# Performance work log

Measured on AMD Instinct MI355X. Metric: run time of the kernel, lower is better.

Reference implementation:

```python
import jax, jax.numpy as jnp
import numpy as np
from jax import lax

IMG = 256; STRIDE = 16; FH = FW = 16; A = 9
SCALES = (32.0, 64.0, 128.0); RATIOS = (0.5, 1.0, 2.0)
N_PROP = 2000; CROP = 14
C_BB = 64


def _conv(x, w, b, stride=1, pad='SAME'):
    y = lax.conv_general_dilated(x, w, (stride, stride), pad,
                                 dimension_numbers=('NCHW', 'OIHW', 'NCHW'))
    return y + b[None, :, None, None]


def _anchors():
    s = jnp.array(SCALES, jnp.float32); r = jnp.array(RATIOS, jnp.float32)
    sr = jnp.stack(jnp.meshgrid(s, r, indexing='ij'), -1).reshape(-1, 2)  # [A,2]
    ws = sr[:, 0] * jnp.sqrt(sr[:, 1]); hs = sr[:, 0] / jnp.sqrt(sr[:, 1])
    cy = (jnp.arange(FH, dtype=jnp.float32) + 0.5) * STRIDE
    cx = (jnp.arange(FW, dtype=jnp.float32) + 0.5) * STRIDE
    cy, cx = jnp.meshgrid(cy, cx, indexing='ij')
    cy = cy[..., None]; cx = cx[..., None]  # [FH,FW,1]
    return jnp.stack([cx - ws / 2, cy - hs / 2, cx + ws / 2, cy + hs / 2], -1).reshape(-1, 4)


def _decode(deltas, anchors):
    w = anchors[:, 2] - anchors[:, 0]; h = anchors[:, 3] - anchors[:, 1]
    cx = anchors[:, 0] + 0.5 * w; cy = anchors[:, 1] + 0.5 * h
    ncx = cx + deltas[:, 0] * w; ncy = cy + deltas[:, 1] * h
    nw = w * jnp.exp(deltas[:, 2]); nh = h * jnp.exp(deltas[:, 3])
    return jnp.stack([ncx - 0.5 * nw, ncy - 0.5 * nh, ncx + 0.5 * nw, ncy + 0.5 * nh], -1)


def _clip(b):
    lim = jnp.float32(IMG - 1)
    return jnp.stack([jnp.clip(b[:, 0], 0, lim), jnp.clip(b[:, 1], 0, lim),
                      jnp.clip(b[:, 2], 0, lim), jnp.clip(b[:, 3], 0, lim)], -1)


def _nms(boxes, scores, thr):
    # greedy NMS; returns order (desc score) and keep mask in sorted order
    order = jnp.argsort(-scores)
    b = boxes[order]
    area = jnp.maximum(b[:, 2] - b[:, 0], 0) * jnp.maximum(b[:, 3] - b[:, 1], 0)
    xx1 = jnp.maximum(b[:, None, 0], b[None, :, 0]); yy1 = jnp.maximum(b[:, None, 1], b[None, :, 1])
    xx2 = jnp.minimum(b[:, None, 2], b[None, :, 2]); yy2 = jnp.minimum(b[:, None, 3], b[None, :, 3])
    inter = jnp.maximum(xx2 - xx1, 0) * jnp.maximum(yy2 - yy1, 0)
    iou = inter / (area[:, None] + area[None, :] - inter + 1e-8)
    n = boxes.shape[0]; idx = jnp.arange(n)
    def body(i, keep):
        return keep & ~(keep[i] & (iou[i] > thr) & (idx > i))
    keep = lax.fori_loop(0, n, body, jnp.ones(n, dtype=bool))
    return order, keep


def _crop_resize(feat, nboxes):
    # feat [C,FH,FW]; nboxes [N,4] normalized (y1,x1,y2,x2) -> [N,C,CROP,CROP]
    t = jnp.arange(CROP, dtype=jnp.float32) / (CROP - 1)
    def one(bx):
        y1, x1, y2, x2 = bx
        fy = (y1 + (y2 - y1) * t) * (FH - 1)
        fx = (x1 + (x2 - x1) * t) * (FW - 1)
        y0 = jnp.clip(jnp.floor(fy), 0, FH - 1).astype(jnp.int32); y1i = jnp.clip(y0 + 1, 0, FH - 1)
        x0 = jnp.clip(jnp.floor(fx), 0, FW - 1).astype(jnp.int32); x1i = jnp.clip(x0 + 1, 0, FW - 1)
        wy = (fy - y0.astype(fy.dtype))[:, None]   # [CROP,1]
        wx = (fx - x0.astype(fx.dtype))[None, :]   # [1,CROP]
        g = lambda yi, xi: feat[:, yi[:, None], xi[None, :]]  # [C,CROP,CROP]
        top = g(y0, x0) * (1 - wx) + g(y0, x1i) * wx
        bot = g(y1i, x0) * (1 - wx) + g(y1i, x1i) * wx
        return top * (1 - wy) + bot * wy
    return jax.vmap(one)(nboxes)


def _forward(x, w_bb, b_bb, w_rpn, b_rpn, w_cls, b_cls, w_box, b_box,
             w_fc1, b_fc1, w_fc2, b_fc2, w_rcls, b_rcls, w_rbox, b_rbox,
             w_m1, b_m1, w_m2, b_m2):
    anchors = _anchors()
    feat = jax.nn.relu(_conv(x, w_bb, b_bb, stride=STRIDE, pad='VALID'))  # [1,C,16,16]
    h = jax.nn.relu(_conv(feat, w_rpn, b_rpn))
    rpn_logits = _conv(h, w_cls, b_cls)[0].reshape(A, 2, FH, FW).transpose(2, 3, 0, 1).reshape(-1, 2)
    rpn_deltas = _conv(h, w_box, b_box)[0].reshape(A, 4, FH, FW).transpose(2, 3, 0, 1).reshape(-1, 4)
    scores = jax.nn.softmax(rpn_logits, -1)[:, 1]
    boxes = _clip(_decode(rpn_deltas, anchors))
    order, keep = _nms(boxes, scores, 0.5)
    n = boxes.shape[0]
    prio = jnp.where(keep, 0, 1) * n + jnp.arange(n)   # kept first, in score order
    sel = jnp.argsort(prio)[:N_PROP]
    valid = keep[sel]
    proposals = jnp.where(valid[:, None], boxes[order][sel], 0.0)  # [N_PROP,4] xyxy
    nb = jnp.stack([proposals[:, 1], proposals[:, 0], proposals[:, 3], proposals[:, 2]], -1) / (IMG - 1)
    crops = _crop_resize(feat[0], nb)                  # [N_PROP,C,14,14]
    pooled = crops.reshape(N_PROP, C_BB, 7, 2, 7, 2).max(axis=(3, 5))
    flat = pooled.reshape(N_PROP, -1)
    h1 = jax.nn.relu(flat @ w_fc1 + b_fc1)
    h2 = jax.nn.relu(h1 @ w_fc2 + b_fc2)
    rcnn_logits = h2 @ w_rcls + b_rcls                 # [N_PROP,2]
    rcnn_deltas = h2 @ w_rbox + b_rbox                 # [N_PROP,4]
    m = jax.nn.relu(_conv(crops, w_m1, b_m1))
    rcnn_masks = _conv(m, w_m2, b_m2)                  # [N_PROP,1,14,14]
    det_scores = jax.nn.softmax(rcnn_logits, -1)[:, 1]
    dets = _clip(_decode(rcnn_deltas, proposals))
    s2 = jnp.where(valid, det_scores, -1.0)
    order2, keep2 = _nms(dets, s2, 0.3)
    keep2 = keep2 & valid[order2]
    final_dets = jnp.where(keep2[:, None], dets[order2], 0.0)
    final_scores = jnp.where(keep2, det_scores[order2], 0.0)
    final_masks = jax.nn.sigmoid(rcnn_masks[order2][:, 0]) * keep2[:, None, None].astype(crops.dtype)
    return (rpn_logits, rpn_deltas, proposals, anchors, rcnn_logits, rcnn_deltas,
            rcnn_masks, final_dets, final_masks, final_scores, keep2)


def setup_inputs() -> dict:
    key = jax.random.key(0)
    ks = jax.random.split(key, 24)
    rn = lambda k, sh, s: jax.random.normal(k, sh, dtype=jnp.float32) * s
    C = C_BB
    return {
        'x': rn(ks[0], (1, 3, IMG, IMG), 1.0),
        'w_bb': rn(ks[1], (C, 3, STRIDE, STRIDE), 0.03), 'b_bb': jnp.zeros((C,), jnp.float32),
        'w_rpn': rn(ks[2], (C, C, 3, 3), 0.05), 'b_rpn': jnp.zeros((C,), jnp.float32),
        'w_cls': rn(ks[3], (2 * A, C, 1, 1), 0.05), 'b_cls': jnp.zeros((2 * A,), jnp.float32),
        'w_box': rn(ks[4], (4 * A, C, 1, 1), 0.05), 'b_box': jnp.zeros((4 * A,), jnp.float32),
        'w_fc1': rn(ks[5], (C * 7 * 7, 512), 0.02), 'b_fc1': jnp.zeros((512,), jnp.float32),
        'w_fc2': rn(ks[6], (512, 512), 0.04), 'b_fc2': jnp.zeros((512,), jnp.float32),
        'w_rcls': rn(ks[7], (512, 2), 0.05), 'b_rcls': jnp.zeros((2,), jnp.float32),
        'w_rbox': rn(ks[8], (512, 4), 0.05), 'b_rbox': jnp.zeros((4,), jnp.float32),
        'w_m1': rn(ks[9], (C, C, 3, 3), 0.05), 'b_m1': jnp.zeros((C,), jnp.float32),
        'w_m2': rn(ks[10], (1, C, 1, 1), 0.05), 'b_m2': jnp.zeros((1,), jnp.float32),
    }


def reference(x, w_bb, b_bb, w_rpn, b_rpn, w_cls, b_cls, w_box, b_box,
              w_fc1, b_fc1, w_fc2, b_fc2, w_rcls, b_rcls, w_rbox, b_rbox,
              w_m1, b_m1, w_m2, b_m2):
    return _forward(x, w_bb, b_bb, w_rpn, b_rpn, w_cls, b_cls, w_box, b_box,
                    w_fc1, b_fc1, w_fc2, b_fc2, w_rcls, b_rcls, w_rbox, b_rbox,
                    w_m1, b_m1, w_m2, b_m2)
```

## Files before the change

### kernel.cpp

```cpp
#include <hip/hip_runtime.h>
#include <math.h>

typedef unsigned long long u64;
typedef unsigned short u16;
typedef __attribute__((ext_vector_type(8))) short bf16x8;
typedef __attribute__((ext_vector_type(4))) float f32x4;
typedef __attribute__((ext_vector_type(16))) float f32x16;

#define N_ANCH 2304
#define NP     2000
#define W1     36
#define W2     32

#define O_RPN_LOGITS   0
#define O_RPN_DELTAS   4608
#define O_PROPOSALS    13824
#define O_ANCHORS      21824
#define O_RCNN_LOGITS  31040
#define O_RCNN_DELTAS  35040
#define O_RCNN_MASKS   43040
#define O_FINAL_DETS   435040
#define O_FINAL_MASKS  443040
#define O_FINAL_SCORES 835040
#define O_KEEP2        837040

__device__ __forceinline__ u16 f2bf(float f) {
    unsigned int x = __float_as_uint(f);
    unsigned int r = x + 0x7fffu + ((x >> 16) & 1u);
    return (u16)(r >> 16);
}

__global__ __launch_bounds__(256) void bb_conv(const float* __restrict__ x,
    const float* __restrict__ w, const float* __restrict__ b,
    float* __restrict__ feat, float* __restrict__ feat_tf)
{
    __shared__ __align__(16) float ws_[768];
    int c = blockIdx.x;
    for (int e = threadIdx.x; e < 192; e += 256)
        ((float4*)ws_)[e] = ((const float4*)(w + c*768))[e];
    __syncthreads();
    int fy = threadIdx.x >> 4, fx = threadIdx.x & 15;
    float acc = b[c];
    for (int ic = 0; ic < 3; ++ic)
        for (int ky = 0; ky < 16; ++ky) {
            const float* xr = x + (size_t)(ic*256 + fy*16+ky)*256 + fx*16;
            const float* wr = ws_ + ic*256 + ky*16;
            float xv[16];
            *(float4*)&xv[0]  = *(const float4*)(xr);
            *(float4*)&xv[4]  = *(const float4*)(xr+4);
            *(float4*)&xv[8]  = *(const float4*)(xr+8);
            *(float4*)&xv[12] = *(const float4*)(xr+12);
            #pragma unroll
            for (int kx = 0; kx < 16; ++kx) acc += xv[kx]*wr[kx];
        }
    float v = fmaxf(acc, 0.f);
    feat[c*256 + threadIdx.x] = v;
    feat_tf[threadIdx.x*64 + c] = v;
}

__global__ __launch_bounds__(256) void rpn_conv(const float* __restrict__ feat,
    const float* __restrict__ w, const float* __restrict__ b, float* __restrict__ h)
{
    __shared__ __align__(16) float f[16384];
    __shared__ __align__(16) float ws_[576];
    int c = blockIdx.x;
    for (int e = threadIdx.x; e < 4096; e += 256)
        ((float4*)f)[e] = ((const float4*)feat)[e];
    for (int e = threadIdx.x; e < 144; e += 256)
        ((float4*)ws_)[e] = ((const float4*)(w + c*576))[e];
    __syncthreads();
    int fy = threadIdx.x >> 4, fx = threadIdx.x & 15;
    float acc = b[c];
    for (int ic = 0; ic < 64; ++ic) {
        const float* fc = f + ic*256;
        const float* wc = ws_ + ic*9;
        #pragma unroll
        for (int dy = 0; dy < 3; ++dy) {
            int y = fy + dy - 1;
            if (y < 0 || y > 15) continue;
            #pragma unroll
            for (int dx = 0; dx < 3; ++dx) {
                int xx = fx + dx - 1;
                if (xx < 0 || xx > 15) continue;
                acc += fc[y*16+xx]*wc[dy*3+dx];
            }
        }
    }
    h[c*256 + threadIdx.x] = fmaxf(acc, 0.f);
}

__global__ __launch_bounds__(256) void heads_rpn(const float* __restrict__ hbuf,
    const float* __restrict__ w_cls, const float* __restrict__ b_cls,
    const float* __restrict__ w_box, const float* __restrict__ b_box,
    float* __restrict__ out_logits, float* __restrict__ out_deltas,
    float* __restrict__ out_anchors,
    float* __restrict__ scores, float* __restrict__ boxes)
{
    int idx = blockIdx.x*256 + threadIdx.x;
    if (idx >= N_ANCH) return;
    int fy = idx / 144, r = idx % 144, fx = r / 9, a = r % 9;
    int pix = fy*16 + fx;
    float l0 = b_cls[a*2+0], l1 = b_cls[a*2+1];
    float d0 = b_box[a*4+0], d1 = b_box[a*4+1], d2 = b_box[a*4+2], d3 = b_box[a*4+3];
    const float* wc0 = w_cls + (a*2+0)*64;
    const float* wc1 = w_cls + (a*2+1)*64;
    const float* wb0 = w_box + (a*4+0)*64;
    const float* wb1 = w_box + (a*4+1)*64;
    const float* wb2 = w_box + (a*4+2)*64;
    const float* wb3 = w_box + (a*4+3)*64;
    for (int c = 0; c < 64; ++c) {
        float hv = hbuf[c*256 + pix];
        l0 += hv*wc0[c]; l1 += hv*wc1[c];
        d0 += hv*wb0[c]; d1 += hv*wb1[c]; d2 += hv*wb2[c]; d3 += hv*wb3[c];
    }
    out_logits[idx*2+0] = l0; out_logits[idx*2+1] = l1;
    out_deltas[idx*4+0] = d0; out_deltas[idx*4+1] = d1;
    out_deltas[idx*4+2] = d2; out_deltas[idx*4+3] = d3;
    float mx = fmaxf(l0,l1);
    float e0 = expf(l0-mx), e1 = expf(l1-mx);
    scores[idx] = e1/(e0+e1);
    float SC = (a/3 == 0) ? 32.f : ((a/3 == 1) ? 64.f : 128.f);
    float RT = (a%3 == 0) ? 0.5f : ((a%3 == 1) ? 1.f : 2.f);
    float wsz = SC*sqrtf(RT), hsz = SC/sqrtf(RT);
    float cx = (fx+0.5f)*16.f, cy = (fy+0.5f)*16.f;
    float ax1 = cx - wsz*0.5f, ay1 = cy - hsz*0.5f;
    float ax2 = cx + wsz*0.5f, ay2 = cy + hsz*0.5f;
    out_anchors[idx*4+0]=ax1; out_anchors[idx*4+1]=ay1;
    out_anchors[idx*4+2]=ax2; out_anchors[idx*4+3]=ay2;
    float aw = ax2-ax1, ah = ay2-ay1;
    float acx = ax1 + 0.5f*aw, acy = ay1 + 0.5f*ah;
    float ncx = acx + d0*aw, ncy = acy + d1*ah;
    float nw = aw*expf(d2), nh = ah*expf(d3);
    float x1 = ncx - 0.5f*nw, y1 = ncy - 0.5f*nh;
    float x2 = ncx + 0.5f*nw, y2 = ncy + 0.5f*nh;
    const float lim = 255.f;
    x1 = fminf(fmaxf(x1,0.f),lim); y1 = fminf(fmaxf(y1,0.f),lim);
    x2 = fminf(fmaxf(x2,0.f),lim); y2 = fminf(fmaxf(y2,0.f),lim);
    boxes[idx*4+0]=x1; boxes[idx*4+1]=y1; boxes[idx*4+2]=x2; boxes[idx*4+3]=y2;
}

__global__ __launch_bounds__(256) void rank_part(const float* __restrict__ score,
    int* __restrict__ parts, int n)
{
    __shared__ __align__(16) float sj[256];
    int it = blockIdx.x, jt = blockIdx.y;
    int i = it*256 + threadIdx.x;
    int j0 = jt*256;
    int jj = j0 + threadIdx.x;
    sj[threadIdx.x] = (jj < n) ? score[jj] : 0.f;
    __syncthreads();
    if (i >= n) return;
    float si = score[i];
    int jmax = min(256, n - j0);
    int cnt = 0;
    const float4* s4 = (const float4*)sj;
    int q4 = jmax >> 2;
    for (int q = 0; q < q4; ++q) {
        float4 v = s4[q];
        int j = j0 + q*4;
        cnt += (v.x > si) || (v.x == si && (j+0) < i);
        cnt += (v.y > si) || (v.y == si && (j+1) < i);
        cnt += (v.z > si) || (v.z == si && (j+2) < i);
        cnt += (v.w > si) || (v.w == si && (j+3) < i);
    }
    parts[(size_t)jt*n + i] = cnt;
}

__global__ __launch_bounds__(256) void rank_scatter(const int* __restrict__ parts,
    int* __restrict__ order, int n, int S)
{
    int i = blockIdx.x*256 + threadIdx.x;
    if (i >= n) return;
    int r = 0;
    for (int s = 0; s < S; ++s) r += parts[(size_t)s*n + i];
    order[r] = i;
}

__global__ __launch_bounds__(256) void gather_sorted(const float4* __restrict__ boxes,
    const int* __restrict__ order, float4* __restrict__ sb, float* __restrict__ sa, int n)
{
    int i = blockIdx.x*256 + threadIdx.x;
    if (i >= n) return;
    float4 b = boxes[order[i]];
    sb[i] = b;
    sa[i] = fmaxf(b.z-b.x, 0.f)*fmaxf(b.w-b.y, 0.f);
}

__global__ __launch_bounds__(256) void iou_mask(const float4* __restrict__ sb,
    const float* __restrict__ sa, int n, int ntotal, int words, float thr,
    u64* __restrict__ mask)
{
    int gid = blockIdx.x*256 + threadIdx.x;
    if (gid >= ntotal*words) return;
    int i = gid / words, w = gid % words;
    if (i >= n) { mask[(size_t)i*words + w] = 0; return; }
    float4 bi = sb[i]; float ai = sa[i];
    u64 m = 0;
    int j0 = w*64;
    for (int bb = 0; bb < 64; ++bb) {
        int j = j0 + bb;
        if (j > i && j < n) {
            float4 bj = sb[j];
            float xx1 = fmaxf(bi.x, bj.x), yy1 = fmaxf(bi.y, bj.y);
            float xx2 = fminf(bi.z, bj.z), yy2 = fminf(bi.w, bj.w);
            float inter = fmaxf(xx2-xx1, 0.f)*fmaxf(yy2-yy1, 0.f);
            float iou = inter / (ai + sa[j] - inter + 1e-8f);
            if (iou > thr) m |= 1ULL << bb;
        }
    }
    mask[(size_t)i*words + w] = m;
}

__global__ __launch_bounds__(256, 1) void nms_scan_wg(const u64* __restrict__ mask,
    int nblk, int words, u64* __restrict__ remout)
{
    __shared__ u64 rem_lds[64];
    __shared__ u64 diagS[64];
    __shared__ u64 pslot[8*64];
    int t = threadIdx.x;
    int ngrp = 256 / words;
    int g = t / words, c = t % words;
    bool pactive = (g < ngrp);
    int gg = min(g, ngrp - 1);
    if (t < 64) {
        rem_lds[t] = ~0ULL;
        diagS[t] = mask[(size_t)t*words + 0];
    }
    __syncthreads();
    for (int b = 0; b < nblk; ++b) {
        const u64* blockbase = mask + (size_t)(64*b)*words;
        u64 vals[10];
        int rows[10];
        #pragma unroll
        for (int k = 0; k < 10; ++k) {
            int r = min(gg + k*ngrp, 63);
            rows[k] = r;
            vals[k] = blockbase[(size_t)r*words + c];
        }
        u64 dnext = mask[(size_t)(64*(b+1) + (t & 63))*words + min(b+1, words-1)];
        u64 mydia = diagS[t & 63];
        u64 nz = __ballot(mydia != 0ULL);
        u64 cur = rem_lds[b];
        u64 pend = cur & nz;
        unsigned mlo = (unsigned)mydia;
        unsigned mhi = (unsigned)(mydia >> 32);
        while (pend) {
            int i = __ffsll((unsigned long long)pend) - 1;
            unsigned lo = __builtin_amdgcn_readlane((int)mlo, i);
            unsigned hi = __builtin_amdgcn_readlane((int)mhi, i);
            u64 dia = ((u64)hi << 32) | lo;
            cur  &= ~dia;
            pend &= ~dia;
            pend &= pend - 1;
        }
        u64 partial = ~0ULL;
        #pragma unroll
        for (int k = 0; k < 10; ++k) {
            bool al = (cur >> rows[k]) & 1ULL;
            partial &= al ? ~vals[k] : ~0ULL;
        }
        if (pactive) pslot[g*64 + c] = partial;
        __syncthreads();
        if (t < 64) diagS[t] = dnext;
        if (t < words) {
            u64 red = rem_lds[t];
            for (int g2 = 0; g2 < ngrp; ++g2) red &= pslot[g2*64 + t];
            rem_lds[t] = red;
        }
        __syncthreads();
    }
    if (t < words) remout[t] = rem_lds[t];
}

__global__ __launch_bounds__(256) void select_props(const u64* __restrict__ remw,
    const float4* __restrict__ sboxes, float* __restrict__ prop_out,
    float4* __restrict__ propws, int* __restrict__ validat, int* __restrict__ kcnt)
{
    __shared__ int cnt[256];
    __shared__ int pref[257];
    int t = threadIdx.x;
    int base = t*9;
    int c = 0;
    #pragma unroll
    for (int q = 0; q < 9; ++q) { int i = base+q; c += (int)((remw[i>>6]>>(i&63))&1ULL); }
    cnt[t] = c; __syncthreads();
    if (t == 0) { pref[0]=0; for (int u=0;u<256;u++) pref[u+1]=pref[u]+cnt[u]; }
    __syncthreads();
    int K = pref[256];
    if (t == 0) kcnt[0] = K;
    int kb = pref[t];
    int nb = K + (base - pref[t]);
    for (int q = 0; q < 9; ++q) {
        int i = base + q;
        int k = (int)((remw[i>>6]>>(i&63))&1ULL);
        int pos = k ? kb : nb;
        if (k) kb++; else nb++;
        if (pos < NP) {
            validat[pos] = k;
            float4 p = k ? sboxes[i] : make_float4(0.f,0.f,0.f,0.f);
            propws[pos] = p;
            prop_out[pos*4+0]=p.x; prop_out[pos*4+1]=p.y;
            prop_out[pos*4+2]=p.z; prop_out[pos*4+3]=p.w;
        }
    }
}

__global__ __launch_bounds__(256) void prep_wbt(const float* __restrict__ w, u16* __restrict__ wbt)
{
    int e = blockIdx.x*256 + threadIdx.x;
    if (e >= 36864) return;
    int oc = e / 576, rem = e % 576, ic = rem / 9, tap = rem % 9;
    int kg = ic >> 4, half = (ic >> 3) & 1, el = ic & 7;
    wbt[((tap*4 + kg)*2 + half)*512 + oc*8 + el] = f2bf(w[e]);
}

__global__ __launch_bounds__(256, 3) void mask_head_fused(const float* __restrict__ feat_tf,
    const float4* __restrict__ propws, const u16* __restrict__ wbt,
    const float* __restrict__ b_m1, const float* __restrict__ w_m2,
    const float* __restrict__ b_m2, float* __restrict__ masks_out,
    float* __restrict__ flat, const int* __restrict__ kcnt)
{
    __shared__ __align__(16) u16 crop[256*64];
    __shared__ unsigned pooled[3136];
    __shared__ __align__(16) int4 cidx[196];
    __shared__ float2 cwt[196];
    __shared__ int2 cmeta[196];
    __shared__ __align__(16) float wm2s[64];
    __shared__ __align__(16) float b1s[64];
    int n = blockIdx.x;
    if (n > *kcnt) return;
    int t = threadIdx.x;
    float4 p = propws[n];

    #pragma unroll
    for (int k = 0; k < 8; ++k)
        *(int4*)(crop + k*2048 + t*8) = make_int4(0,0,0,0);
    for (int e = t; e < 3136; e += 256) pooled[e] = 0;
    if (t < 64) { wm2s[t] = w_m2[t]; b1s[t] = b_m1[t]; }
    if (t < 196) {
        float x1n = p.x*(1.f/255.f), y1n = p.y*(1.f/255.f);
        float x2n = p.z*(1.f/255.f), y2n = p.w*(1.f/255.f);
        int py = t / 14, px = t - py*14;
        float fyv = (y1n + (y2n-y1n)*(py*(1.f/13.f)))*15.f;
        float fxv = (x1n + (x2n-x1n)*(px*(1.f/13.f)))*15.f;
        int y0 = min(max((int)floorf(fyv),0),15), y1i = min(y0+1,15);
        int x0 = min(max((int)floorf(fxv),0),15), x1i = min(x0+1,15);
        float wy = fyv - (float)y0, wx = fxv - (float)x0;
        cidx[t] = make_int4((y0*16+x0)*64, (y0*16+x1i)*64, (y1i*16+x0)*64, (y1i*16+x1i)*64);
        cwt[t] = make_float2(wy, wx);
        cmeta[t] = make_int2((py+1)*16 + px + 1, (py>>1)*7 + (px>>1));
    }
    __syncthreads();

    int wave = t >> 6, lane = t & 63;
    for (int it = 0; it < 49; ++it) {
        int idx = it*4 + wave;
        int4 o4 = cidx[idx];
        float2 w2 = cwt[idx];
        int2 mt = cmeta[idx];
        float v00 = feat_tf[o4.x + lane];
        float v01 = feat_tf[o4.y + lane];
        float v10 = feat_tf[o4.z + lane];
        float v11 = feat_tf[o4.w + lane];
        float wy = w2.x, wx = w2.y;
        float top = v00*(1.f-wx) + v01*wx;
        float bot = v10*(1.f-wx) + v11*wx;
        float val = top*(1.f-wy) + bot*wy;
        int g = mt.x;
        crop[g*64 + (((lane>>3) ^ (g&7))<<3) + (lane&7)] = f2bf(val);
        atomicMax(&pooled[lane*49 + mt.y], __float_as_uint(val));
    }
    __syncthreads();

    {
        size_t rowoff = (size_t)n*3136;
        for (int k = t; k < 3136; k += 256)
            flat[rowoff + k] = __uint_as_float(pooled[k]);
    }

    int l31 = lane & 31, half = lane >> 5;
    int pix0 = wave*64 + l31, pix1 = pix0 + 32;

    f32x16 acc[2][2];
    #pragma unroll
    for (int o = 0; o < 2; ++o) {
        #pragma unroll
        for (int q = 0; q < 4; ++q) {
            float4 b4 = *(const float4*)&b1s[o*32 + 4*half + 8*q];
            #pragma unroll
            for (int pp = 0; pp < 2; ++pp) {
                acc[pp][o][q*4+0] = b4.x; acc[pp][o][q*4+1] = b4.y;
                acc[pp][o][q*4+2] = b4.z; acc[pp][o][q*4+3] = b4.w;
            }
        }
    }

    for (int tap = 0; tap < 9; ++tap) {
        int doff = (tap/3 - 1)*16 + (tap%3) - 1;
        int p0 = (pix0 + doff) & 255;
        int p1 = (pix1 + doff) & 255;
        const u16* wt = wbt + tap*4096;
        bf16x8 af[2][4];
        #pragma unroll
        for (int kg = 0; kg < 4; ++kg) {
            #pragma unroll
            for (int o = 0; o < 2; ++o)
                af[o][kg] = *(const bf16x8*)(wt + (kg*2 + half)*512 + (o*32 + l31)*8);
        }
        int x0v = p0&7, x1v = p1&7;
        #pragma unroll
        for (int kg = 0; kg < 4; ++kg) {
            int slot = kg*2 + half;
            bf16x8 bf0 = *(const bf16x8*)(crop + p0*64 + ((slot ^ x0v)<<3));
            bf16x8 bf1 = *(const bf16x8*)(crop + p1*64 + ((slot ^ x1v)<<3));
            acc[0][0] = __builtin_amdgcn_mfma_f32_32x32x16_bf16(af[0][kg], bf0, acc[0][0], 0, 0, 0);
            acc[0][1] = __builtin_amdgcn_mfma_f32_32x32x16_bf16(af[1][kg], bf0, acc[0][1], 0, 0, 0);
            acc[1][0] = __builtin_amdgcn_mfma_f32_32x32x16_bf16(af[0][kg], bf1, acc[1][0], 0, 0, 0);
            acc[1][1] = __builtin_amdgcn_mfma_f32_32x32x16_bf16(af[1][kg], bf1, acc[1][1], 0, 0, 0);
        }
    }

    float4 wmq[2][4];
    #pragma unroll
    for (int o = 0; o < 2; ++o)
        #pragma unroll
        for (int q = 0; q < 4; ++q)
            wmq[o][q] = *(const float4*)&wm2s[o*32 + 4*half + 8*q];
    float s0 = 0.f, s1 = 0.f;
    #pragma unroll
    for (int o = 0; o < 2; ++o) {
        #pragma unroll
        for (int q = 0; q < 4; ++q) {
            float4 w4 = wmq[o][q];
            s0 = fmaf(fmaxf(acc[0][o][q*4+0], 0.f), w4.x, s0);
            s0 = fmaf(fmaxf(acc[0][o][q*4+1], 0.f), w4.y, s0);
            s0 = fmaf(fmaxf(acc[0][o][q*4+2], 0.f), w4.z, s0);
            s0 = fmaf(fmaxf(acc[0][o][q*4+3], 0.f), w4.w, s0);
            s1 = fmaf(fmaxf(acc[1][o][q*4+0], 0.f), w4.x, s1);
            s1 = fmaf(fmaxf(acc[1][o][q*4+1], 0.f), w4.y, s1);
            s1 = fmaf(fmaxf(acc[1][o][q*4+2], 0.f), w4.z, s1);
            s1 = fmaf(fmaxf(acc[1][o][q*4+3], 0.f), w4.w, s1);
        }
    }
    s0 += __shfl_xor(s0, 32);
    s1 += __shfl_xor(s1, 32);
    float sv = (half ? s1 : s0) + b_m2[0];
    int pw = half ? pix1 : pix0;
    int pyy = (pw>>4) - 1, pxx = (pw&15) - 1;
    if ((unsigned)pyy < 14u && (unsigned)pxx < 14u)
        masks_out[(size_t)n*196 + pyy*14 + pxx] = sv;
}

__global__ __launch_bounds__(256) void bcast_rows(const int* __restrict__ kcnt,
    float* __restrict__ out_logits, float* __restrict__ out_deltas,
    float* __restrict__ masks_out, float4* __restrict__ dets,
    float* __restrict__ dscores, float* __restrict__ s2)
{
    int K = *kcnt;
    int j = blockIdx.x;
    if (j <= K) return;
    int t = threadIdx.x;
    if (t < 196) {
        masks_out[(size_t)j*196 + t] = masks_out[(size_t)K*196 + t];
    } else if (t == 196) {
        out_logits[j*2+0] = out_logits[K*2+0];
        out_logits[j*2+1] = out_logits[K*2+1];
    } else if (t == 197) {
        out_deltas[j*4+0] = out_deltas[K*4+0];
        out_deltas[j*4+1] = out_deltas[K*4+1];
        out_deltas[j*4+2] = out_deltas[K*4+2];
        out_deltas[j*4+3] = out_deltas[K*4+3];
    } else if (t == 198) {
        dets[j] = dets[K];
        dscores[j] = dscores[K];
        s2[j] = s2[K];
    }
}

__global__ __launch_bounds__(64) void gemm_f32_w1(const float* __restrict__ A,
    const float* __restrict__ B, float* __restrict__ Cpart,
    int M, int N, int K, int Kblk, const int* __restrict__ kcnt)
{
    int flat = blockIdx.x + blockIdx.y*gridDim.x;
    int colt = ((flat & 7) << 1) | ((flat >> 3) & 1);
    int rowt = flat >> 4;
    int row0 = rowt*32, col0 = colt*32;
    if (row0 > *kcnt) return;
    __shared__ __align__(16) float As[32][36];
    __shared__ __align__(16) float Bs[32][36];
    int s = blockIdx.z;
    int kbase = s*Kblk;
    int t = threadIdx.x;

    int arow = t >> 1;
    int kh   = (t & 1) * 16;
    int am = min(row0 + arow, M-1);
    const float* Arow = A + (size_t)am*K + kbase + kh;
    int bk = t & 31;
    int ch = (t >> 5) * 16;
    const float* Bbase = B + (size_t)(kbase + bk)*N + col0 + ch;

    int cx = t & 7, ry = (t >> 3) & 7;
    int rbase = ry*4, cbase = cx*4;

    float4 pa0 = *(const float4*)(Arow);
    float4 pa1 = *(const float4*)(Arow + 4);
    float4 pa2 = *(const float4*)(Arow + 8);
    float4 pa3 = *(const float4*)(Arow + 12);
    float4 pb0 = *(const float4*)(Bbase);
    float4 pb1 = *(const float4*)(Bbase + 4);
    float4 pb2 = *(const float4*)(Bbase + 8);
    float4 pb3 = *(const float4*)(Bbase + 12);

    float acc[4][4] = {};
    for (int k0 = 0; k0 < Kblk; k0 += 32) {
        As[kh+ 0][arow]=pa0.x; As[kh+ 1][arow]=pa0.y; As[kh+ 2][arow]=pa0.z; As[kh+ 3][arow]=pa0.w;
        As[kh+ 4][arow]=pa1.x; As[kh+ 5][arow]=pa1.y; As[kh+ 6][arow]=pa1.z; As[kh+ 7][arow]=pa1.w;
        As[kh+ 8][arow]=pa2.x; As[kh+ 9][arow]=pa2.y; As[kh+10][arow]=pa2.z; As[kh+11][arow]=pa2.w;
        As[kh+12][arow]=pa3.x; As[kh+13][arow]=pa3.y; As[kh+14][arow]=pa3.z; As[kh+15][arow]=pa3.w;
        *(float4*)&Bs[bk][ch]    = pb0;
        *(float4*)&Bs[bk][ch+4]  = pb1;
        *(float4*)&Bs[bk][ch+8]  = pb2;
        *(float4*)&Bs[bk][ch+12] = pb3;
        __syncthreads();
        int kn = k0 + 32;
        if (kn < Kblk) {
            pa0 = *(const float4*)(Arow + kn);
            pa1 = *(const float4*)(Arow + kn + 4);
            pa2 = *(const float4*)(Arow + kn + 8);
            pa3 = *(const float4*)(Arow + kn + 12);
            const float* Bn = Bbase + (size_t)kn*N;
            pb0 = *(const float4*)(Bn);
            pb1 = *(const float4*)(Bn + 4);
            pb2 = *(const float4*)(Bn + 8);
            pb3 = *(const float4*)(Bn + 12);
        }
        #pragma unroll
        for (int k = 0; k < 32; ++k) {
            float4 av = *(float4*)&As[k][rbase];
            float4 bv = *(float4*)&Bs[k][cbase];
            float a_[4] = {av.x, av.y, av.z, av.w};
            float b_[4] = {bv.x, bv.y, bv.z, bv.w};
            #pragma unroll
            for (int i = 0; i < 4; ++i)
                #pragma unroll
                for (int j = 0; j < 4; ++j)
                    acc[i][j] = fmaf(a_[i], b_[j], acc[i][j]);
        }
        __syncthreads();
    }
    float* Cp = Cpart + (size_t)s*M*N;
    #pragma unroll
    for (int i = 0; i < 4; ++i) {
        int gm = row0 + rbase + i;
        if (gm >= M) continue;
        #pragma unroll
        for (int j = 0; j < 4; ++j) {
            int gn = col0 + cbase + j;
            Cp[(size_t)gm*N + gn] = acc[i][j];
        }
    }
}

__global__ __launch_bounds__(256) void combine_parts(const float* __restrict__ parts,
    const float* __restrict__ bias, float* __restrict__ C,
    int MN, int N, int S, int relu, const int* __restrict__ kcnt)
{
    int i4 = blockIdx.x*256 + threadIdx.x;
    if (i4*4 >= MN) return;
    size_t idx = (size_t)i4*4;
    if ((int)(idx / (unsigned)N) > *kcnt) return;
    float4 acc = *(const float4*)(parts + idx);
    for (int s = 1; s < S; ++s) {
        float4 v = *(const float4*)(parts + (size_t)s*MN + idx);
        acc.x += v.x; acc.y += v.y; acc.z += v.z; acc.w += v.w;
    }
    int nb = (int)(idx & (N-1));
    float4 bv = *(const float4*)(bias + nb);
    acc.x += bv.x; acc.y += bv.y; acc.z += bv.z; acc.w += bv.w;
    if (relu) {
        acc.x = fmaxf(acc.x, 0.f); acc.y = fmaxf(acc.y, 0.f);
        acc.z = fmaxf(acc.z, 0.f); acc.w = fmaxf(acc.w, 0.f);
    }
    *(float4*)(C + idx) = acc;
}

__global__ __launch_bounds__(256) void rcnn_heads_lds(const float* __restrict__ h2,
    const float* __restrict__ w_rcls, const float* __restrict__ b_rcls,
    const float* __restrict__ w_rbox, const float* __restrict__ b_rbox,
    const float4* __restrict__ propws, const int* __restrict__ validat,
    float* __restrict__ out_logits, float* __restrict__ out_deltas,
    float4* __restrict__ dets, float* __restrict__ dscores, float* __restrict__ s2,
    const int* __restrict__ kcnt)
{
    int b0 = blockIdx.x*8;
    if (b0 > *kcnt) return;
    __shared__ float hs[8*520];
    for (int e = threadIdx.x; e < 8*512; e += 256) {
        int pr = e >> 9, k = e & 511;
        hs[pr*520 + k] = h2[(size_t)(b0+pr)*512 + k];
    }
    __syncthreads();
    int t = threadIdx.x;
    if (t >= 8) return;
    int n = b0 + t;
    const float* hv = hs + t*520;
    float l0 = b_rcls[0], l1 = b_rcls[1];
    float d0 = b_rbox[0], d1 = b_rbox[1], d2 = b_rbox[2], d3 = b_rbox[3];
    for (int k = 0; k < 512; ++k) {
        float v = hv[k];
        l0 = fmaf(v, w_rcls[k*2+0], l0); l1 = fmaf(v, w_rcls[k*2+1], l1);
        d0 = fmaf(v, w_rbox[k*4+0], d0); d1 = fmaf(v, w_rbox[k*4+1], d1);
        d2 = fmaf(v, w_rbox[k*4+2], d2); d3 = fmaf(v, w_rbox[k*4+3], d3);
    }
    out_logits[n*2+0]=l0; out_logits[n*2+1]=l1;
    out_deltas[n*4+0]=d0; out_deltas[n*4+1]=d1;
    out_deltas[n*4+2]=d2; out_deltas[n*4+3]=d3;
    float mx = fmaxf(l0,l1);
    float e0 = expf(l0-mx), e1 = expf(l1-mx);
    float sc = e1/(e0+e1);
    float4 p = propws[n];
    float w = p.z-p.x, h = p.w-p.y;
    float cx = p.x + 0.5f*w, cy = p.y + 0.5f*h;
    float ncx = cx + d0*w, ncy = cy + d1*h;
    float nw = w*expf(d2), nh = h*expf(d3);
    float x1 = ncx-0.5f*nw, y1 = ncy-0.5f*nh, x2 = ncx+0.5f*nw, y2 = ncy+0.5f*nh;
    const float lim = 255.f;
    x1 = fminf(fmaxf(x1,0.f),lim); y1 = fminf(fmaxf(y1,0.f),lim);
    x2 = fminf(fmaxf(x2,0.f),lim); y2 = fminf(fmaxf(y2,0.f),lim);
    dets[n] = make_float4(x1,y1,x2,y2);
    dscores[n] = sc;
    s2[n] = validat[n] ? sc : -1.0f;
}

__global__ void finalize(const u64* __restrict__ remw2,
    const int* __restrict__ order2, const int* __restrict__ validat,
    const float4* __restrict__ dets, const float* __restrict__ dscores,
    const float* __restrict__ masks_in, float* __restrict__ fdets,
    float* __restrict__ fscores, float* __restrict__ fmasks, float* __restrict__ keep2out)
{
    int j = blockIdx.x;
    int t = threadIdx.x;
    int o = order2[j];
    int kb = (int)((remw2[j>>6] >> (j&63)) & 1ULL);
    int k2 = kb & validat[o];
    if (t == 0) {
        float4 d = dets[o];
        if (!k2) d = make_float4(0.f,0.f,0.f,0.f);
        fdets[j*4+0]=d.x; fdets[j*4+1]=d.y; fdets[j*4+2]=d.z; fdets[j*4+3]=d.w;
        fscores[j] = k2 ? dscores[o] : 0.f;
        keep2out[j] = (float)k2;
    }
    if (t < 196) {
        float mv = masks_in[(size_t)o*196 + t];
        float sg = 1.f/(1.f + expf(-mv));
        fmasks[(size_t)j*196 + t] = k2 ? sg : 0.f;
    }
}

extern "C" void kernel_launch(void* const* d_in, const int* in_sizes, int n_in,
                              void* d_out, int out_size, void* d_ws, size_t ws_size,
                              hipStream_t stream)
{
    const float* x      = (const float*)d_in[0];
    const float* w_bb   = (const float*)d_in[1];
    const float* b_bb   = (const float*)d_in[2];
    const float* w_rpn  = (const float*)d_in[3];
    const float* b_rpn  = (const float*)d_in[4];
    const float* w_cls  = (const float*)d_in[5];
    const float* b_cls  = (const float*)d_in[6];
    const float* w_box  = (const float*)d_in[7];
    const float* b_box  = (const float*)d_in[8];
    const float* w_fc1  = (const float*)d_in[9];
    const float* b_fc1  = (const float*)d_in[10];
    const float* w_fc2  = (const float*)d_in[11];
    const float* b_fc2  = (const float*)d_in[12];
    const float* w_rcls = (const float*)d_in[13];
    const float* b_rcls = (const float*)d_in[14];
    const float* w_rbox = (const float*)d_in[15];
    const float* b_rbox = (const float*)d_in[16];
    const float* w_m1   = (const float*)d_in[17];
    const float* b_m1   = (const float*)d_in[18];
    const float* w_m2   = (const float*)d_in[19];
    const float* b_m2   = (const float*)d_in[20];

    float* out = (float*)d_out;

    char* basep = (char*)d_ws;
    auto alloc = [&](size_t bytes) { char* q = basep; basep += (bytes + 255) & ~(size_t)255; return q; };
    float* feat    = (float*)alloc(16384*4);
    float* feat_tf = (float*)alloc(16384*4);
    float* hbuf    = (float*)alloc(16384*4);
    float* scores  = (float*)alloc(2304*4);
    float* boxes   = (float*)alloc(9216*4);
    int*   order1  = (int*)  alloc(2304*4);
    int*   rparts  = (int*)  alloc((size_t)9*2304*4);
    float* sboxes  = (float*)alloc(9216*4);
    float* sareas  = (float*)alloc(2304*4);
    u64*   supm1   = (u64*)  alloc((size_t)((W1+1)*64)*W1*8);
    u64*   remw1   = (u64*)  alloc(W1*8);
    int*   validat = (int*)  alloc(NP*4);
    float* propws  = (float*)alloc(NP*4*4);
    int*   kcnt    = (int*)  alloc(4);
    u16*   wbt     = (u16*)  alloc(36864*2);
    float* flat    = (float*)alloc((size_t)NP*3136*4);
    float* h1      = (float*)alloc((size_t)NP*512*4);
    float* h2      = (float*)alloc((size_t)NP*512*4);
    float* gparts  = (float*)alloc((size_t)7*NP*512*4);
    float* dets    = (float*)alloc(NP*4*4);
    float* dscores = (float*)alloc(NP*4);
    float* s2      = (float*)alloc(NP*4);
    int*   order2  = (int*)  alloc(NP*4);
    float* sdets   = (float*)alloc(NP*4*4);
    float* sareas2 = (float*)alloc(NP*4);
    u64*   supm2   = (u64*)  alloc((size_t)((W2+1)*64)*W2*8);
    u64*   remw2   = (u64*)  alloc(W2*8);

    bb_conv<<<64, 256, 0, stream>>>(x, w_bb, b_bb, feat, feat_tf);
    rpn_conv<<<64, 256, 0, stream>>>(feat, w_rpn, b_rpn, hbuf);
    heads_rpn<<<9, 256, 0, stream>>>(hbuf, w_cls, b_cls, w_box, b_box,
        out + O_RPN_LOGITS, out + O_RPN_DELTAS, out + O_ANCHORS, scores, boxes);

    rank_part<<<dim3(9, 9), 256, 0, stream>>>(scores, rparts, N_ANCH);
    rank_scatter<<<9, 256, 0, stream>>>(rparts, order1, N_ANCH, 9);
    gather_sorted<<<9, 256, 0, stream>>>((const float4*)boxes, order1,
                                         (float4*)sboxes, sareas, N_ANCH);
    iou_mask<<<(W1*64*W1+255)/256, 256, 0, stream>>>((const float4*)sboxes, sareas,
                                                     N_ANCH, W1*64, W1, 0.5f, supm1);
    nms_scan_wg<<<1, 256, 0, stream>>>(supm1, W1, W1, remw1);
    select_props<<<1, 256, 0, stream>>>(remw1, (const float4*)sboxes,
                                        out + O_PROPOSALS, (float4*)propws, validat, kcnt);

    prep_wbt<<<144, 256, 0, stream>>>(w_m1, wbt);

    mask_head_fused<<<NP, 256, 0, stream>>>(feat_tf, (const float4*)propws, wbt,
        b_m1, w_m2, b_m2, out + O_RCNN_MASKS, flat, kcnt);
    gemm_f32_w1<<<dim3(63, 16, 7), 64, 0, stream>>>(flat, w_fc1, gparts,
                                                    NP, 512, 3136, 448, kcnt);
    combine_parts<<<(NP*512/4+255)/256, 256, 0, stream>>>(gparts, b_fc1, h1,
                                                          NP*512, 512, 7, 1, kcnt);
    gemm_f32_w1<<<dim3(63, 16, 2), 64, 0, stream>>>(h1, w_fc2, gparts,
                                                    NP, 512, 512, 256, kcnt);
    combine_parts<<<(NP*512/4+255)/256, 256, 0, stream>>>(gparts, b_fc2, h2,
                                                          NP*512, 512, 2, 1, kcnt);
    rcnn_heads_lds<<<250, 256, 0, stream>>>(h2, w_rcls, b_rcls, w_rbox, b_rbox,
        (const float4*)propws, validat, out + O_RCNN_LOGITS, out + O_RCNN_DELTAS,
        (float4*)dets, dscores, s2, kcnt);

    bcast_rows<<<NP, 256, 0, stream>>>(kcnt, out + O_RCNN_LOGITS, out + O_RCNN_DELTAS,
        out + O_RCNN_MASKS, (float4*)dets, dscores, s2);

    rank_part<<<dim3(8, 8), 256, 0, stream>>>(s2, rparts, NP);
    rank_scatter<<<8, 256, 0, stream>>>(rparts, order2, NP, 8);
    gather_sorted<<<8, 256, 0, stream>>>((const float4*)dets, order2,
                                         (float4*)sdets, sareas2, NP);
    iou_mask<<<(W2*64*W2+255)/256, 256, 0, stream>>>((const float4*)sdets, sareas2,
                                                     NP, W2*64, W2, 0.3f, supm2);
    nms_scan_wg<<<1, 256, 0, stream>>>(supm2, W2, W2, remw2);
    finalize<<<NP, 256, 0, stream>>>(remw2, order2, validat, (const float4*)dets,
        dscores, out + O_RCNN_MASKS, out + O_FINAL_DETS, out + O_FINAL_SCORES,
        out + O_FINAL_MASKS, out + O_KEEP2);
}
```

Measured before the change: 436.2 us.

## Split RPN conv by row bands, stage head weights in LDS, fuse rank scatter/gather

The RPN 3x3 conv now runs on 64x4 blocks of 64 threads, and each block loads only a 6-row halo band of the feature map instead of the full 64 KB map. This raises parallelism and cuts LDS staging. heads_rpn uses smaller blocks and reads the classifier and box weights from LDS. rank_scatter and gather_sorted are merged into one kernel that writes sorted boxes directly by rank, removing a launch and an indirect load. iou_mask removes its per-iteration branch with clamped loads and unrolls the loop, at the cost of some redundant arithmetic.

```diff
diff --git a/kernel.cpp b/kernel.cpp
--- a/kernel.cpp
+++ b/kernel.cpp
@@ -58,56 +58,71 @@
     feat_tf[threadIdx.x*64 + c] = v;
 }
 
-__global__ __launch_bounds__(256) void rpn_conv(const float* __restrict__ feat,
+__global__ __launch_bounds__(64) void rpn_conv(const float* __restrict__ feat,
     const float* __restrict__ w, const float* __restrict__ b, float* __restrict__ h)
 {
-    __shared__ __align__(16) float f[16384];
+    __shared__ __align__(16) float fl[64*6*16];
     __shared__ __align__(16) float ws_[576];
     int c = blockIdx.x;
-    for (int e = threadIdx.x; e < 4096; e += 256)
-        ((float4*)f)[e] = ((const float4*)feat)[e];
-    for (int e = threadIdx.x; e < 144; e += 256)
+    int q = blockIdx.y;
+    int r0 = q*4;
+    int t = threadIdx.x;
+    for (int e = t; e < 144; e += 64)
         ((float4*)ws_)[e] = ((const float4*)(w + c*576))[e];
-    __syncthreads();
-    int fy = threadIdx.x >> 4, fx = threadIdx.x & 15;
+    for (int e = t; e < 1536; e += 64) {
+        int ic = e / 24, rem = e % 24, sl = rem >> 2, xq = rem & 3;
+        int yg = r0 - 1 + sl;
+        if ((unsigned)yg < 16u)
+            ((float4*)fl)[ic*24 + sl*4 + xq] = ((const float4*)feat)[ic*64 + yg*4 + xq];
+    }
+    __syncthreads();
+    int p = q*64 + t;
+    int fy = p >> 4, fx = p & 15;
     float acc = b[c];
     for (int ic = 0; ic < 64; ++ic) {
-        const float* fc = f + ic*256;
+        const float* fc = fl + ic*96;
         const float* wc = ws_ + ic*9;
         #pragma unroll
         for (int dy = 0; dy < 3; ++dy) {
             int y = fy + dy - 1;
             if (y < 0 || y > 15) continue;
+            int sl = y - (r0 - 1);
             #pragma unroll
             for (int dx = 0; dx < 3; ++dx) {
                 int xx = fx + dx - 1;
                 if (xx < 0 || xx > 15) continue;
-                acc += fc[y*16+xx]*wc[dy*3+dx];
+                acc += fc[sl*16 + xx]*wc[dy*3 + dx];
             }
         }
     }
-    h[c*256 + threadIdx.x] = fmaxf(acc, 0.f);
-}
-
-__global__ __launch_bounds__(256) void heads_rpn(const float* __restrict__ hbuf,
+    h[c*256 + p] = fmaxf(acc, 0.f);
+}
+
+__global__ __launch_bounds__(64) void heads_rpn(const float* __restrict__ hbuf,
     const float* __restrict__ w_cls, const float* __restrict__ b_cls,
     const float* __restrict__ w_box, const float* __restrict__ b_box,
     float* __restrict__ out_logits, float* __restrict__ out_deltas,
     float* __restrict__ out_anchors,
     float* __restrict__ scores, float* __restrict__ boxes)
 {
-    int idx = blockIdx.x*256 + threadIdx.x;
+    __shared__ __align__(16) float wcs[1152];
+    __shared__ __align__(16) float wbs[2304];
+    int t = threadIdx.x;
+    for (int e = t; e < 288; e += 64) ((float4*)wcs)[e] = ((const float4*)w_cls)[e];
+    for (int e = t; e < 576; e += 64) ((float4*)wbs)[e] = ((const float4*)w_box)[e];
+    __syncthreads();
+    int idx = blockIdx.x*64 + t;
     if (idx >= N_ANCH) return;
     int fy = idx / 144, r = idx % 144, fx = r / 9, a = r % 9;
     int pix = fy*16 + fx;
     float l0 = b_cls[a*2+0], l1 = b_cls[a*2+1];
     float d0 = b_box[a*4+0], d1 = b_box[a*4+1], d2 = b_box[a*4+2], d3 = b_box[a*4+3];
-    const float* wc0 = w_cls + (a*2+0)*64;
-    const float* wc1 = w_cls + (a*2+1)*64;
-    const float* wb0 = w_box + (a*4+0)*64;
-    const float* wb1 = w_box + (a*4+1)*64;
-    const float* wb2 = w_box + (a*4+2)*64;
-    const float* wb3 = w_box + (a*4+3)*64;
+    const float* wc0 = wcs + (a*2+0)*64;
+    const float* wc1 = wcs + (a*2+1)*64;
+    const float* wb0 = wbs + (a*4+0)*64;
+    const float* wb1 = wbs + (a*4+1)*64;
+    const float* wb2 = wbs + (a*4+2)*64;
+    const float* wb3 = wbs + (a*4+3)*64;
     for (int c = 0; c < 64; ++c) {
         float hv = hbuf[c*256 + pix];
         l0 += hv*wc0[c]; l1 += hv*wc1[c];
@@ -166,24 +181,18 @@
     parts[(size_t)jt*n + i] = cnt;
 }
 
-__global__ __launch_bounds__(256) void rank_scatter(const int* __restrict__ parts,
-    int* __restrict__ order, int n, int S)
+__global__ __launch_bounds__(256) void rank_scatter_gather(const int* __restrict__ parts,
+    const float4* __restrict__ boxes, int* __restrict__ order,
+    float4* __restrict__ sb, float* __restrict__ sa, int n, int S)
 {
     int i = blockIdx.x*256 + threadIdx.x;
     if (i >= n) return;
     int r = 0;
     for (int s = 0; s < S; ++s) r += parts[(size_t)s*n + i];
     order[r] = i;
-}
-
-__global__ __launch_bounds__(256) void gather_sorted(const float4* __restrict__ boxes,
-    const int* __restrict__ order, float4* __restrict__ sb, float* __restrict__ sa, int n)
-{
-    int i = blockIdx.x*256 + threadIdx.x;
-    if (i >= n) return;
-    float4 b = boxes[order[i]];
-    sb[i] = b;
-    sa[i] = fmaxf(b.z-b.x, 0.f)*fmaxf(b.w-b.y, 0.f);
+    float4 bx = boxes[i];
+    sb[r] = bx;
+    sa[r] = fmaxf(bx.z-bx.x, 0.f)*fmaxf(bx.w-bx.y, 0.f);
 }
 
 __global__ __launch_bounds__(256) void iou_mask(const float4* __restrict__ sb,
@@ -197,16 +206,17 @@
     float4 bi = sb[i]; float ai = sa[i];
     u64 m = 0;
     int j0 = w*64;
+    #pragma unroll 8
     for (int bb = 0; bb < 64; ++bb) {
         int j = j0 + bb;
-        if (j > i && j < n) {
-            float4 bj = sb[j];
-            float xx1 = fmaxf(bi.x, bj.x), yy1 = fmaxf(bi.y, bj.y);
-            float xx2 = fminf(bi.z, bj.z), yy2 = fminf(bi.w, bj.w);
-            float inter = fmaxf(xx2-xx1, 0.f)*fmaxf(yy2-yy1, 0.f);
-            float iou = inter / (ai + sa[j] - inter + 1e-8f);
-            if (iou > thr) m |= 1ULL << bb;
-        }
+        int jc = min(j, n-1);
+        float4 bj = sb[jc];
+        float aj = sa[jc];
+        float xx1 = fmaxf(bi.x, bj.x), yy1 = fmaxf(bi.y, bj.y);
+        float xx2 = fminf(bi.z, bj.z), yy2 = fminf(bi.w, bj.w);
+        float inter = fmaxf(xx2-xx1, 0.f)*fmaxf(yy2-yy1, 0.f);
+        float iou = inter / (ai + aj - inter + 1e-8f);
+        if (j > i && j < n && iou > thr) m |= 1ULL << bb;
     }
     mask[(size_t)i*words + w] = m;
 }
@@ -717,14 +727,13 @@
     u64*   remw2   = (u64*)  alloc(W2*8);
 
     bb_conv<<<64, 256, 0, stream>>>(x, w_bb, b_bb, feat, feat_tf);
-    rpn_conv<<<64, 256, 0, stream>>>(feat, w_rpn, b_rpn, hbuf);
-    heads_rpn<<<9, 256, 0, stream>>>(hbuf, w_cls, b_cls, w_box, b_box,
+    rpn_conv<<<dim3(64, 4), 64, 0, stream>>>(feat, w_rpn, b_rpn, hbuf);
+    heads_rpn<<<36, 64, 0, stream>>>(hbuf, w_cls, b_cls, w_box, b_box,
         out + O_RPN_LOGITS, out + O_RPN_DELTAS, out + O_ANCHORS, scores, boxes);
 
     rank_part<<<dim3(9, 9), 256, 0, stream>>>(scores, rparts, N_ANCH);
-    rank_scatter<<<9, 256, 0, stream>>>(rparts, order1, N_ANCH, 9);
-    gather_sorted<<<9, 256, 0, stream>>>((const float4*)boxes, order1,
-                                         (float4*)sboxes, sareas, N_ANCH);
+    rank_scatter_gather<<<9, 256, 0, stream>>>(rparts, (const float4*)boxes,
+        order1, (float4*)sboxes, sareas, N_ANCH, 9);
     iou_mask<<<(W1*64*W1+255)/256, 256, 0, stream>>>((const float4*)sboxes, sareas,
                                                      N_ANCH, W1*64, W1, 0.5f, supm1);
     nms_scan_wg<<<1, 256, 0, stream>>>(supm1, W1, W1, remw1);
@@ -751,9 +760,8 @@
         out + O_RCNN_MASKS, (float4*)dets, dscores, s2);
 
     rank_part<<<dim3(8, 8), 256, 0, stream>>>(s2, rparts, NP);
-    rank_scatter<<<8, 256, 0, stream>>>(rparts, order2, NP, 8);
-    gather_sorted<<<8, 256, 0, stream>>>((const float4*)dets, order2,
-                                         (float4*)sdets, sareas2, NP);
+    rank_scatter_gather<<<8, 256, 0, stream>>>(rparts, (const float4*)dets,
+        order2, (float4*)sdets, sareas2, NP, 8);
     iou_mask<<<(W2*64*W2+255)/256, 256, 0, stream>>>((const float4*)sdets, sareas2,
                                                      NP, W2*64, W2, 0.3f, supm2);
     nms_scan_wg<<<1, 256, 0, stream>>>(supm2, W2, W2, remw2);
```

New measurement: 439.7 us. Within noise of the previous version (+0.8%).
